# Optimization experiments

Measured on AMD Instinct MI355X. Metric: run time of the kernel, lower is better.

## Reference

```python
import jax, jax.numpy as jnp
import numpy as np

E = 1_000_000   # number of multicut edges
T = 2_000_000   # number of triplets (GNN nodes)
M = 4_000_000   # number of directed GNN edges among triplets
HID = 32


def gcn_conv(x, edge_index, W, b, n):
    """PyG GCNConv: x' = D^-1/2 (A+I) D^-1/2 (x W) + b, symmetric norm with self-loops."""
    src, dst = edge_index[0], edge_index[1]
    xw = x @ W                                        # [n, out]
    deg = jnp.zeros((n,), xw.dtype).at[dst].add(1.0) + 1.0  # +1 self-loop
    dis = jax.lax.rsqrt(deg)                          # deg^-1/2
    norm = dis[src] * dis[dst]                        # [M]
    msg = xw[src] * norm[:, None]                     # gather + scale
    out = jax.ops.segment_sum(msg, dst, num_segments=n)
    out = out + xw * (dis * dis)[:, None]             # self-loop contribution
    return out + b


def setup_inputs() -> dict:
    key = jax.random.key(0)
    ks = jax.random.split(key, 16)
    inp = {
        "edge_costs": jax.random.normal(ks[0], (E,), jnp.float32),
        "t12": jax.random.normal(ks[1], (T,), jnp.float32),
        "t13": jax.random.normal(ks[2], (T,), jnp.float32),
        "t23": jax.random.normal(ks[3], (T,), jnp.float32),
        "corr_12": jax.random.randint(ks[4], (T,), 0, E),
        "corr_13": jax.random.randint(ks[5], (T,), 0, E),
        "corr_23": jax.random.randint(ks[6], (T,), 0, E),
        # counts >= 1 so the divide is well-defined (as in real triplet decompositions)
        "edge_counter": jax.random.randint(ks[7], (E,), 1, 6).astype(jnp.float32),
        "edge_index": jax.random.randint(ks[8], (2, M), 0, T),
        # GCNConv / Linear parameters (glorot-ish scale)
        "W1": jax.random.normal(ks[9], (3, HID), jnp.float32) * (1.0 / np.sqrt(3)),
        "b1": jnp.zeros((HID,), jnp.float32),
        "W2": jax.random.normal(ks[10], (HID, HID), jnp.float32) * (1.0 / np.sqrt(HID)),
        "b2": jnp.zeros((HID,), jnp.float32),
        "Wout": jax.random.normal(ks[11], (HID, 3), jnp.float32) * (1.0 / np.sqrt(HID)),
        "bout": jnp.zeros((3,), jnp.float32),
    }
    return inp


def reference(edge_costs, t12, t13, t23, corr_12, corr_13, corr_23,
              edge_counter, edge_index, W1, b1, W2, b2, Wout, bout):
    # --- send_messages_to_triplets: gather / divide, then zero covered edges ---
    t12 = t12 + edge_costs[corr_12] / edge_counter[corr_12]
    t13 = t13 + edge_costs[corr_13] / edge_counter[corr_13]
    t23 = t23 + edge_costs[corr_23] / edge_counter[corr_23]
    edge_costs = jnp.where(edge_counter > 0, jnp.zeros_like(edge_costs), edge_costs)

    # --- send_messages_to_edges: 2-layer GCN over triplet nodes + linear head ---
    tri = jnp.stack([t12, t13, t23], axis=1)          # [T, 3]
    x = jax.nn.relu(gcn_conv(tri, edge_index, W1, b1, T))
    x = jax.nn.relu(gcn_conv(x, edge_index, W2, b2, T))
    delta = x @ Wout + bout                           # [T, 3]

    t12 = t12 - delta[:, 0]
    t13 = t13 - delta[:, 1]
    t23 = t23 - delta[:, 2]

    edge_updates = (jnp.zeros_like(edge_costs)
                    .at[corr_12].add(delta[:, 0])
                    .at[corr_13].add(delta[:, 1])
                    .at[corr_23].add(delta[:, 2]))
    edge_costs = edge_costs + edge_updates
    return (edge_costs, t12, t13, t23)
```

## Files before the change

### kernel.cpp

```cpp
#include <hip/hip_runtime.h>
#include <hip/hip_fp16.h>
#include <math.h>

#define HID 32
#define BS 256

#define NPB 4096
#define NBK_MAX 1024
#define EBT 8192
#define CAP 11776

typedef _Float16 h2v __attribute__((ext_vector_type(2)));

__device__ __forceinline__ h2v u2h(uint u) { return __builtin_bit_cast(h2v, u); }
__device__ __forceinline__ uint h2u(h2v h) { return __builtin_bit_cast(uint, h); }
__device__ __forceinline__ uint pack2(float a, float b) {
  h2v r; r.x = (_Float16)a; r.y = (_Float16)b; return h2u(r);
}
__device__ __forceinline__ float dot2acc(uint a, uint b, float c) {
#if __has_builtin(__builtin_amdgcn_fdot2)
  return __builtin_amdgcn_fdot2(u2h(a), u2h(b), c, false);
#else
  h2v ah = u2h(a), bh = u2h(b);
  c = fmaf((float)ah.x, (float)bh.x, c);
  return fmaf((float)ah.y, (float)bh.y, c);
#endif
}
__device__ __forceinline__ float h4w(uint2 g) {
  h2v hi = u2h(g.y); return (float)hi.y;
}


__global__ void k_zero_i(int* __restrict__ p, int n) {
  int i = blockIdx.x * BS + threadIdx.x;
  if (i < n) p[i] = 0;
}


__global__ __launch_bounds__(BS) void k_bhist(const int* __restrict__ ei,
                                              int* __restrict__ gh, int M, int NBK) {
  __shared__ int hist[NBK_MAX];
  for (int b = threadIdx.x; b < NBK; b += BS) hist[b] = 0;
  __syncthreads();
  int e0 = blockIdx.x * EBT;
  int n = min(EBT, M - e0);
  for (int k = threadIdx.x; k < n; k += BS) {
    int d = ei[M + e0 + k];
    atomicAdd(&hist[d / NPB], 1);
  }
  __syncthreads();
  for (int b = threadIdx.x; b < NBK; b += BS)
    if (hist[b]) atomicAdd(&gh[b], hist[b]);
}


__global__ __launch_bounds__(BS) void k_bscan(const int* __restrict__ gh,
                                              int* __restrict__ gboff,
                                              int* __restrict__ gcur, int NBK) {
  __shared__ int part[BS];
  int C = (NBK + BS - 1) / BS;
  int s = 0;
  for (int k = 0; k < C; ++k) {
    int idx = threadIdx.x * C + k;
    if (idx < NBK) s += gh[idx];
  }
  part[threadIdx.x] = s;
  __syncthreads();
  for (int off = 1; off < BS; off <<= 1) {
    int v = part[threadIdx.x];
    int u = (threadIdx.x >= off) ? part[threadIdx.x - off] : 0;
    __syncthreads();
    part[threadIdx.x] = v + u;
    __syncthreads();
  }
  int run = (threadIdx.x > 0) ? part[threadIdx.x - 1] : 0;
  for (int k = 0; k < C; ++k) {
    int idx = threadIdx.x * C + k;
    if (idx < NBK) {
      gboff[idx] = run;
      gcur[idx] = run;
      run += gh[idx];
    }
  }
  if (threadIdx.x == BS - 1) gboff[NBK] = run;
}


__global__ __launch_bounds__(BS) void k_bscatter(const int* __restrict__ ei,
                                                 int* __restrict__ gcur,
                                                 int2* __restrict__ P, int M, int NBK) {
  __shared__ int hist[NBK_MAX];
  __shared__ int excl[NBK_MAX];
  __shared__ int curs[NBK_MAX];
  __shared__ int base[NBK_MAX];
  __shared__ int part[BS];
  for (int b = threadIdx.x; b < NBK; b += BS) hist[b] = 0;
  __syncthreads();
  int e0 = blockIdx.x * EBT;
  int n = min(EBT, M - e0);
  for (int k = threadIdx.x; k < n; k += BS) {
    int d = ei[M + e0 + k];
    atomicAdd(&hist[d / NPB], 1);
  }
  __syncthreads();
  int C = (NBK + BS - 1) / BS;
  int s = 0;
  for (int k = 0; k < C; ++k) {
    int idx = threadIdx.x * C + k;
    if (idx < NBK) s += hist[idx];
  }
  part[threadIdx.x] = s;
  __syncthreads();
  for (int off = 1; off < BS; off <<= 1) {
    int v = part[threadIdx.x];
    int u = (threadIdx.x >= off) ? part[threadIdx.x - off] : 0;
    __syncthreads();
    part[threadIdx.x] = v + u;
    __syncthreads();
  }
  int run = (threadIdx.x > 0) ? part[threadIdx.x - 1] : 0;
  for (int k = 0; k < C; ++k) {
    int idx = threadIdx.x * C + k;
    if (idx < NBK) {
      excl[idx] = run;
      curs[idx] = run;
      run += hist[idx];
    }
  }
  __syncthreads();
  for (int b = threadIdx.x; b < NBK; b += BS)
    base[b] = hist[b] ? atomicAdd(&gcur[b], hist[b]) : 0;
  __syncthreads();
  for (int k = threadIdx.x; k < n; k += BS) {
    int sidx = ei[e0 + k];
    int d = ei[M + e0 + k];
    int b = d / NPB;
    int pos = atomicAdd(&curs[b], 1);
    int gpos = base[b] + (pos - excl[b]);
    P[gpos] = make_int2(sidx, d);
  }
}


__global__ __launch_bounds__(BS) void k_bfinal(const int2* __restrict__ P,
                                               const int* __restrict__ gboff,
                                               int* __restrict__ row_ptr,
                                               int* __restrict__ srt, int T, int M,
                                               int NBK) {
  __shared__ int cnt[NPB];
  __shared__ int lsrt[CAP];
  __shared__ int part[BS];
  int b = blockIdx.x;
  int d0 = b * NPB;
  int nodesHere = min(NPB, T - d0);
  int p0 = gboff[b], p1 = gboff[b + 1];
  int nE = p1 - p0;
  for (int j = threadIdx.x; j < NPB; j += BS) cnt[j] = 0;
  __syncthreads();
  for (int j = threadIdx.x; j < nE; j += BS) {
    int2 p = P[p0 + j];
    atomicAdd(&cnt[p.y - d0], 1);
  }
  __syncthreads();
  const int CN = NPB / BS;
  int s = 0;
#pragma unroll
  for (int k = 0; k < CN; ++k) s += cnt[threadIdx.x * CN + k];
  part[threadIdx.x] = s;
  __syncthreads();
  for (int off = 1; off < BS; off <<= 1) {
    int v = part[threadIdx.x];
    int u = (threadIdx.x >= off) ? part[threadIdx.x - off] : 0;
    __syncthreads();
    part[threadIdx.x] = v + u;
    __syncthreads();
  }
  int run = (threadIdx.x > 0) ? part[threadIdx.x - 1] : 0;
#pragma unroll
  for (int k = 0; k < CN; ++k) {
    int idx = threadIdx.x * CN + k;
    int c = cnt[idx];
    cnt[idx] = run;
    if (idx < nodesHere) row_ptr[d0 + idx] = p0 + run;
    run += c;
  }
  if (b == NBK - 1 && threadIdx.x == 0) row_ptr[T] = M;
  __syncthreads();
  if (nE <= CAP) {
    for (int j = threadIdx.x; j < nE; j += BS) {
      int2 p = P[p0 + j];
      int pos = atomicAdd(&cnt[p.y - d0], 1);
      lsrt[pos] = p.x;
    }
    __syncthreads();
    for (int j = threadIdx.x; j < nE; j += BS) srt[p0 + j] = lsrt[j];
  } else {
    for (int j = threadIdx.x; j < nE; j += BS) {
      int2 p = P[p0 + j];
      int pos = atomicAdd(&cnt[p.y - d0], 1);
      srt[p0 + pos] = p.x;
    }
  }
}


__global__ void k_prep_e(const float* __restrict__ ec, const float* __restrict__ cnt,
                         float* __restrict__ msg, float* __restrict__ oec, int E) {
  int i = blockIdx.x * BS + threadIdx.x;
  if (i >= E) return;
  float c = cnt[i], v = ec[i];
  msg[i] = v / c;
  oec[i] = (c > 0.0f) ? 0.0f : v;
}

__global__ void k_step1pack(const float* __restrict__ msg,
                            const float* __restrict__ t12, const float* __restrict__ t13,
                            const float* __restrict__ t23,
                            const int* __restrict__ c12, const int* __restrict__ c13,
                            const int* __restrict__ c23,
                            const int* __restrict__ row_ptr,
                            float4* __restrict__ tri4, uint2* __restrict__ trih, int T) {
  int i = blockIdx.x * BS + threadIdx.x;
  if (i >= T) return;
  int a = c12[i], b = c13[i], c = c23[i];
  float4 v;
  v.x = t12[i] + msg[a];
  v.y = t13[i] + msg[b];
  v.z = t23[i] + msg[c];
  v.w = rsqrtf((float)(row_ptr[i + 1] - row_ptr[i]) + 1.0f);
  tri4[i] = v;
  uint2 h;
  h.x = pack2(v.x, v.y);
  h.y = pack2(v.z, v.w);
  trih[i] = h;
}

__global__ void k_packw(const float* __restrict__ W1, const float* __restrict__ b1,
                        const float* __restrict__ W2, uint* __restrict__ pkw) {
  int i = blockIdx.x * BS + threadIdx.x;
  if (i < 48) {
    int r = i >> 4, k = i & 15;
    pkw[i] = pack2(W1[r * HID + 2 * k], W1[r * HID + 2 * k + 1]);
  } else if (i < 64) {
    int k = i - 48;
    pkw[i] = pack2(b1[2 * k], b1[2 * k + 1]);
  } else if (i < 576) {
    int idx = i - 64;
    int h2 = idx >> 5, j = idx & 31;
    pkw[i] = pack2(W2[(2 * h2) * HID + j], W2[(2 * h2 + 1) * HID + j]);
  }
}

__device__ __forceinline__ void acc3(uint2 g, float di, float& ax, float& ay, float& az) {
  h2v lo = u2h(g.x), hi = u2h(g.y);
  float w = (float)hi.y * di;
  ax = fmaf((float)lo.x, w, ax);
  ay = fmaf((float)lo.y, w, ay);
  az = fmaf((float)hi.x, w, az);
}

__global__ __launch_bounds__(BS) void k_agg1c(const int* __restrict__ row_ptr,
                                              const int* __restrict__ srt,
                                              const float4* __restrict__ tri4,
                                              const uint2* __restrict__ trih,
                                              uint2* __restrict__ G4h, int T) {
  int i = blockIdx.x * BS + threadIdx.x;
  if (i >= T) return;
  int r0 = row_ptr[i], r1 = row_ptr[i + 1];
  float4 ts = tri4[i];
  float di = ts.w;
  float d2 = di * di;
  float ax = ts.x * d2, ay = ts.y * d2, az = ts.z * d2;
  int e = r0;
  for (; e + 4 <= r1; e += 4) {
    int s0 = srt[e + 0];
    int s1 = srt[e + 1];
    int s2 = srt[e + 2];
    int s3 = srt[e + 3];
    uint2 g0 = trih[s0];
    uint2 g1 = trih[s1];
    uint2 g2 = trih[s2];
    uint2 g3 = trih[s3];
    acc3(g0, di, ax, ay, az);
    acc3(g1, di, ax, ay, az);
    acc3(g2, di, ax, ay, az);
    acc3(g3, di, ax, ay, az);
  }
  for (; e < r1; ++e) {
    uint2 g = trih[srt[e]];
    acc3(g, di, ax, ay, az);
  }
  uint2 o;
  o.x = pack2(ax, ay);
  o.y = pack2(az, di);
  G4h[i] = o;
}

__device__ __forceinline__ void edge_h1_accu(uint2 g, float w,
                                             const uint* __restrict__ W1s,
                                             const uint* __restrict__ b1s,
                                             float* S) {
  h2v lo = u2h(g.x), hi = u2h(g.y);
  h2v hx; hx.x = lo.x; hx.y = lo.x;
  h2v hy; hy.x = lo.y; hy.y = lo.y;
  h2v hz; hz.x = hi.x; hz.y = hi.x;
  h2v zero; zero.x = (_Float16)0.f; zero.y = (_Float16)0.f;
#pragma unroll
  for (int k = 0; k < 16; ++k) {
    h2v t = hx * u2h(W1s[k]) + (hy * u2h(W1s[16 + k]) + (hz * u2h(W1s[32 + k]) + u2h(b1s[k])));
    t = __builtin_elementwise_max(t, zero);
    S[2 * k]     = fmaf((float)t.x, w, S[2 * k]);
    S[2 * k + 1] = fmaf((float)t.y, w, S[2 * k + 1]);
  }
}

__global__ __launch_bounds__(BS, 4) void k_l2head(
    const int* __restrict__ row_ptr, const int* __restrict__ srt,
    const uint2* __restrict__ G4h, const float4* __restrict__ tri4,
    const uint* __restrict__ pkw,
    const float* __restrict__ b2,
    const float* __restrict__ Wout, const float* __restrict__ bout,
    const int* __restrict__ c12, const int* __restrict__ c13,
    const int* __restrict__ c23,
    float* __restrict__ o12, float* __restrict__ o13, float* __restrict__ o23,
    float* __restrict__ oec, int T) {
  int i = blockIdx.x * BS + threadIdx.x;
  if (i >= T) return;
  int r0 = row_ptr[i], r1 = row_ptr[i + 1];
  uint2 gs = G4h[i];
  float4 tp = tri4[i];
  float di = tp.w;
  const uint* W1s = pkw;
  const uint* b1s = pkw + 48;
  const uint* W2s = pkw + 64;

  float S[HID];
#pragma unroll
  for (int h = 0; h < HID; ++h) S[h] = 0.0f;

  edge_h1_accu(gs, di * di, W1s, b1s, S);

  int e = r0;
  for (; e + 4 <= r1; e += 4) {
    int s0 = srt[e + 0];
    int s1 = srt[e + 1];
    int s2 = srt[e + 2];
    int s3 = srt[e + 3];
    uint2 g0 = G4h[s0];
    uint2 g1 = G4h[s1];
    uint2 g2 = G4h[s2];
    uint2 g3 = G4h[s3];
    float w0 = h4w(g0) * di;
    float w1 = h4w(g1) * di;
    float w2 = h4w(g2) * di;
    float w3 = h4w(g3) * di;
    edge_h1_accu(g0, w0, W1s, b1s, S);
    edge_h1_accu(g1, w1, W1s, b1s, S);
    edge_h1_accu(g2, w2, W1s, b1s, S);
    edge_h1_accu(g3, w3, W1s, b1s, S);
  }
  if (e + 2 <= r1) {
    int s0 = srt[e + 0];
    int s1 = srt[e + 1];
    uint2 g0 = G4h[s0];
    uint2 g1 = G4h[s1];
    float w0 = h4w(g0) * di;
    float w1 = h4w(g1) * di;
    edge_h1_accu(g0, w0, W1s, b1s, S);
    edge_h1_accu(g1, w1, W1s, b1s, S);
    e += 2;
  }
  if (e < r1) {
    uint2 g = G4h[srt[e]];
    edge_h1_accu(g, h4w(g) * di, W1s, b1s, S);
  }

  uint sh[16];
#pragma unroll
  for (int k = 0; k < 16; ++k) sh[k] = pack2(S[2 * k], S[2 * k + 1]);

  float d0 = bout[0], d1 = bout[1], dd2 = bout[2];
#pragma unroll
  for (int cz = 0; cz < 4; ++cz) {
    float z[8];
#pragma unroll
    for (int j = 0; j < 8; ++j) z[j] = b2[cz * 8 + j];
#pragma unroll
    for (int h2 = 0; h2 < 16; ++h2) {
#pragma unroll
      for (int j = 0; j < 8; ++j)
        z[j] = dot2acc(sh[h2], W2s[h2 * HID + cz * 8 + j], z[j]);
    }
#pragma unroll
    for (int j = 0; j < 8; ++j) {
      float v = fmaxf(z[j], 0.0f);
      int jp = cz * 8 + j;
      d0  = fmaf(v, Wout[jp * 3 + 0], d0);
      d1  = fmaf(v, Wout[jp * 3 + 1], d1);
      dd2 = fmaf(v, Wout[jp * 3 + 2], dd2);
    }
  }

  o12[i] = tp.x - d0;
  o13[i] = tp.y - d1;
  o23[i] = tp.z - dd2;
  unsafeAtomicAdd(&oec[c12[i]], d0);
  unsafeAtomicAdd(&oec[c13[i]], d1);
  unsafeAtomicAdd(&oec[c23[i]], dd2);
}


extern "C" void kernel_launch(void* const* d_in, const int* in_sizes, int n_in,
                              void* d_out, int out_size, void* d_ws, size_t ws_size,
                              hipStream_t stream) {
  const float* ec  = (const float*)d_in[0];
  const float* t12 = (const float*)d_in[1];
  const float* t13 = (const float*)d_in[2];
  const float* t23 = (const float*)d_in[3];
  const int* c12   = (const int*)d_in[4];
  const int* c13   = (const int*)d_in[5];
  const int* c23   = (const int*)d_in[6];
  const float* cnt = (const float*)d_in[7];
  const int* ei    = (const int*)d_in[8];
  const float* W1  = (const float*)d_in[9];
  const float* b1  = (const float*)d_in[10];
  const float* W2  = (const float*)d_in[11];
  const float* b2  = (const float*)d_in[12];
  const float* Wout = (const float*)d_in[13];
  const float* bout = (const float*)d_in[14];

  const int E = in_sizes[0];
  const int T = in_sizes[1];
  const int M = in_sizes[8] / 2;
  const int NBK = (T + NPB - 1) / NPB;

  float* oec = (float*)d_out;
  float* o12 = oec + E;
  float* o13 = o12 + T;
  float* o23 = o13 + T;

  float4* tri4 = (float4*)d_ws;
  uint2*  trih = (uint2*)(tri4 + T);
  uint2*  G4h  = trih + T;
  int*    srt  = (int*)(G4h + T);
  int*    rptr = srt + M;
  float*  msg  = (float*)(rptr + (T + 1));
  int*    gh   = (int*)(msg + E);
  int*    gboff = gh + NBK;
  int*    gcur  = gboff + (NBK + 1);
  uint*   pkw   = (uint*)(gcur + NBK);
  int2*   P    = (int2*)tri4;

  auto blocks = [](long n) { return (int)((n + BS - 1) / BS); };
  const int tiles = (M + EBT - 1) / EBT;

  k_zero_i<<<blocks(NBK), BS, 0, stream>>>(gh, NBK);
  k_bhist<<<tiles, BS, 0, stream>>>(ei, gh, M, NBK);
  k_bscan<<<1, BS, 0, stream>>>(gh, gboff, gcur, NBK);
  k_bscatter<<<tiles, BS, 0, stream>>>(ei, gcur, P, M, NBK);
  k_bfinal<<<NBK, BS, 0, stream>>>(P, gboff, rptr, srt, T, M, NBK);

  k_packw<<<3, BS, 0, stream>>>(W1, b1, W2, pkw);
  k_prep_e<<<blocks(E), BS, 0, stream>>>(ec, cnt, msg, oec, E);
  k_step1pack<<<blocks(T), BS, 0, stream>>>(msg, t12, t13, t23, c12, c13, c23,
                                            rptr, tri4, trih, T);

  k_agg1c<<<blocks(T), BS, 0, stream>>>(rptr, srt, tri4, trih, G4h, T);

  k_l2head<<<blocks(T), BS, 0, stream>>>(rptr, srt, G4h, tri4, pkw,
                                         b2, Wout, bout,
                                         c12, c13, c23, o12, o13, o23, oec, T);
}
```

Baseline: 709.1 us.

## Replace global atomic edge scatter with bucketed sort and shared-memory segment sum

The per-triplet global float atomics into the edge cost array are removed. The head kernel now writes deltas to a buffer, and the 3T (edge, triplet) pairs are bucket-sorted by edge index into 1024-edge bins. A new kernel then gathers and accumulates each bin with shared-memory atomics and does a single coalesced add into the output. This adds four extra launches plus histogram and scatter passes over 6M keys, and the launch-bounds occupancy hint on the head kernel is dropped.

```diff
diff --git a/kernel.cpp b/kernel.cpp
--- a/kernel.cpp
+++ b/kernel.cpp
@@ -9,6 +9,8 @@
 #define NBK_MAX 1024
 #define EBT 8192
 #define CAP 11776
+
+#define NPB_E 1024
 
 typedef _Float16 h2v __attribute__((ext_vector_type(2)));
 
@@ -201,6 +203,121 @@
       srt[p0 + pos] = p.x;
     }
   }
+}
+
+
+__global__ __launch_bounds__(BS) void k_ehist(const int* __restrict__ c12,
+                                              const int* __restrict__ c13,
+                                              const int* __restrict__ c23,
+                                              int* __restrict__ gh, int T, int NBK) {
+  __shared__ int hist[NBK_MAX];
+  for (int b = threadIdx.x; b < NBK; b += BS) hist[b] = 0;
+  __syncthreads();
+  int N3 = 3 * T;
+  int j0 = blockIdx.x * EBT;
+  int n = min(EBT, N3 - j0);
+  for (int k = threadIdx.x; k < n; k += BS) {
+    int j = j0 + k;
+    int key = (j < T) ? c12[j] : ((j < 2 * T) ? c13[j - T] : c23[j - 2 * T]);
+    atomicAdd(&hist[key / NPB_E], 1);
+  }
+  __syncthreads();
+  for (int b = threadIdx.x; b < NBK; b += BS)
+    if (hist[b]) atomicAdd(&gh[b], hist[b]);
+}
+
+__global__ __launch_bounds__(BS) void k_escatter(const int* __restrict__ c12,
+                                                 const int* __restrict__ c13,
+                                                 const int* __restrict__ c23,
+                                                 int* __restrict__ gcur,
+                                                 int2* __restrict__ PE, int T, int NBK) {
+  __shared__ int hist[NBK_MAX];
+  __shared__ int excl[NBK_MAX];
+  __shared__ int curs[NBK_MAX];
+  __shared__ int base[NBK_MAX];
+  __shared__ int part[BS];
+  for (int b = threadIdx.x; b < NBK; b += BS) hist[b] = 0;
+  __syncthreads();
+  int N3 = 3 * T;
+  int j0 = blockIdx.x * EBT;
+  int n = min(EBT, N3 - j0);
+  for (int k = threadIdx.x; k < n; k += BS) {
+    int j = j0 + k;
+    int key = (j < T) ? c12[j] : ((j < 2 * T) ? c13[j - T] : c23[j - 2 * T]);
+    atomicAdd(&hist[key / NPB_E], 1);
+  }
+  __syncthreads();
+  int C = (NBK + BS - 1) / BS;
+  int s = 0;
+  for (int k = 0; k < C; ++k) {
+    int idx = threadIdx.x * C + k;
+    if (idx < NBK) s += hist[idx];
+  }
+  part[threadIdx.x] = s;
+  __syncthreads();
+  for (int off = 1; off < BS; off <<= 1) {
+    int v = part[threadIdx.x];
+    int u = (threadIdx.x >= off) ? part[threadIdx.x - off] : 0;
+    __syncthreads();
+    part[threadIdx.x] = v + u;
+    __syncthreads();
+  }
+  int run = (threadIdx.x > 0) ? part[threadIdx.x - 1] : 0;
+  for (int k = 0; k < C; ++k) {
+    int idx = threadIdx.x * C + k;
+    if (idx < NBK) {
+      excl[idx] = run;
+      curs[idx] = run;
+      run += hist[idx];
+    }
+  }
+  __syncthreads();
+  for (int b = threadIdx.x; b < NBK; b += BS)
+    base[b] = hist[b] ? atomicAdd(&gcur[b], hist[b]) : 0;
+  __syncthreads();
+  for (int k = threadIdx.x; k < n; k += BS) {
+    int j = j0 + k;
+    int key = (j < T) ? c12[j] : ((j < 2 * T) ? c13[j - T] : c23[j - 2 * T]);
+    int b = key / NPB_E;
+    int pos = atomicAdd(&curs[b], 1);
+    int gpos = base[b] + (pos - excl[b]);
+    PE[gpos] = make_int2(key, j);
+  }
+}
+
+__global__ __launch_bounds__(BS) void k_oecsum(const int2* __restrict__ PE,
+                                               const int* __restrict__ gboff,
+                                               const float* __restrict__ dd,
+                                               float* __restrict__ oec, int E) {
+  __shared__ float acc[NPB_E];
+  int b = blockIdx.x;
+  int e0 = b * NPB_E;
+  int p0 = gboff[b], p1 = gboff[b + 1];
+  int n = p1 - p0;
+  for (int j = threadIdx.x; j < NPB_E; j += BS) acc[j] = 0.0f;
+  __syncthreads();
+  int k = threadIdx.x;
+  for (; k + 3 * BS < n; k += 4 * BS) {
+    int2 q0 = PE[p0 + k];
+    int2 q1 = PE[p0 + k + BS];
+    int2 q2 = PE[p0 + k + 2 * BS];
+    int2 q3 = PE[p0 + k + 3 * BS];
+    float v0 = dd[q0.y];
+    float v1 = dd[q1.y];
+    float v2 = dd[q2.y];
+    float v3 = dd[q3.y];
+    atomicAdd(&acc[q0.x - e0], v0);
+    atomicAdd(&acc[q1.x - e0], v1);
+    atomicAdd(&acc[q2.x - e0], v2);
+    atomicAdd(&acc[q3.x - e0], v3);
+  }
+  for (; k < n; k += BS) {
+    int2 q = PE[p0 + k];
+    atomicAdd(&acc[q.x - e0], dd[q.y]);
+  }
+  __syncthreads();
+  int lim = min(NPB_E, E - e0);
+  for (int j = threadIdx.x; j < lim; j += BS) oec[e0 + j] += acc[j];
 }
 
 
@@ -314,16 +431,14 @@
   }
 }
 
-__global__ __launch_bounds__(BS, 4) void k_l2head(
+__global__ __launch_bounds__(BS) void k_l2head(
     const int* __restrict__ row_ptr, const int* __restrict__ srt,
     const uint2* __restrict__ G4h, const float4* __restrict__ tri4,
     const uint* __restrict__ pkw,
     const float* __restrict__ b2,
     const float* __restrict__ Wout, const float* __restrict__ bout,
-    const int* __restrict__ c12, const int* __restrict__ c13,
-    const int* __restrict__ c23,
     float* __restrict__ o12, float* __restrict__ o13, float* __restrict__ o23,
-    float* __restrict__ oec, int T) {
+    float* __restrict__ dd, int T) {
   int i = blockIdx.x * BS + threadIdx.x;
   if (i >= T) return;
   int r0 = row_ptr[i], r1 = row_ptr[i + 1];
@@ -404,9 +519,9 @@
   o12[i] = tp.x - d0;
   o13[i] = tp.y - d1;
   o23[i] = tp.z - dd2;
-  unsafeAtomicAdd(&oec[c12[i]], d0);
-  unsafeAtomicAdd(&oec[c13[i]], d1);
-  unsafeAtomicAdd(&oec[c23[i]], dd2);
+  dd[i] = d0;
+  dd[T + i] = d1;
+  dd[2 * T + i] = dd2;
 }
 
 
@@ -433,6 +548,7 @@
   const int T = in_sizes[1];
   const int M = in_sizes[8] / 2;
   const int NBK = (T + NPB - 1) / NPB;
+  const int NBK_E = (E + NPB_E - 1) / NPB_E;
 
   float* oec = (float*)d_out;
   float* o12 = oec + E;
@@ -442,17 +558,23 @@
   float4* tri4 = (float4*)d_ws;
   uint2*  trih = (uint2*)(tri4 + T);
   uint2*  G4h  = trih + T;
-  int*    srt  = (int*)(G4h + T);
+  int2*   PE   = (int2*)(G4h + T);
+  float*  dd   = (float*)(PE + 3 * (size_t)T);
+  int*    srt  = (int*)(dd + 3 * (size_t)T);
   int*    rptr = srt + M;
   float*  msg  = (float*)(rptr + (T + 1));
   int*    gh   = (int*)(msg + E);
   int*    gboff = gh + NBK;
   int*    gcur  = gboff + (NBK + 1);
   uint*   pkw   = (uint*)(gcur + NBK);
+  int*    gh_e  = (int*)(pkw + 576);
+  int*    gboff_e = gh_e + NBK_E;
+  int*    gcur_e  = gboff_e + (NBK_E + 1);
   int2*   P    = (int2*)tri4;
 
   auto blocks = [](long n) { return (int)((n + BS - 1) / BS); };
-  const int tiles = (M + EBT - 1) / EBT;
+  const int tiles   = (M + EBT - 1) / EBT;
+  const int tiles_e = (3 * T + EBT - 1) / EBT;
 
   k_zero_i<<<blocks(NBK), BS, 0, stream>>>(gh, NBK);
   k_bhist<<<tiles, BS, 0, stream>>>(ei, gh, M, NBK);
@@ -460,6 +582,11 @@
   k_bscatter<<<tiles, BS, 0, stream>>>(ei, gcur, P, M, NBK);
   k_bfinal<<<NBK, BS, 0, stream>>>(P, gboff, rptr, srt, T, M, NBK);
 
+  k_zero_i<<<blocks(NBK_E), BS, 0, stream>>>(gh_e, NBK_E);
+  k_ehist<<<tiles_e, BS, 0, stream>>>(c12, c13, c23, gh_e, T, NBK_E);
+  k_bscan<<<1, BS, 0, stream>>>(gh_e, gboff_e, gcur_e, NBK_E);
+  k_escatter<<<tiles_e, BS, 0, stream>>>(c12, c13, c23, gcur_e, PE, T, NBK_E);
+
   k_packw<<<3, BS, 0, stream>>>(W1, b1, W2, pkw);
   k_prep_e<<<blocks(E), BS, 0, stream>>>(ec, cnt, msg, oec, E);
   k_step1pack<<<blocks(T), BS, 0, stream>>>(msg, t12, t13, t23, c12, c13, c23,
@@ -469,5 +596,7 @@
 
   k_l2head<<<blocks(T), BS, 0, stream>>>(rptr, srt, G4h, tri4, pkw,
                                          b2, Wout, bout,
-                                         c12, c13, c23, o12, o13, o23, oec, T);
-}
+                                         o12, o13, o23, dd, T);
+
+  k_oecsum<<<NBK_E, BS, 0, stream>>>(PE, gboff_e, dd, oec, E);
+}
```

Measured after the change: 718.4 us. About the same (+1.3%).

## Replace global scatter-add atomics with bucketed sort and shared-memory reduction

Applied to the files above, without the earlier changes.

The final edge-cost scatter-add no longer uses random global atomics from the GCN head. The head now writes deltas to a buffer, which is bucket-sorted by edge index using per-tile histograms and then reduced per bucket with shared-memory atomics. The node-sort pipeline is also rebuilt around deterministic per-tile offsets, replacing the global cursor atomics and the zeroing kernel. The launch-bounds occupancy hint on k_l2head is dropped as well. The cost is extra passes over 6M keys and values, several more kernel launches, and more workspace.

```diff
diff --git a/kernel.cpp b/kernel.cpp
--- a/kernel.cpp
+++ b/kernel.cpp
@@ -9,6 +9,8 @@
 #define NBK_MAX 1024
 #define EBT 8192
 #define CAP 11776
+
+#define NPB_E 2048
 
 typedef _Float16 h2v __attribute__((ext_vector_type(2)));
 
@@ -31,14 +33,8 @@
 }
 
 
-__global__ void k_zero_i(int* __restrict__ p, int n) {
-  int i = blockIdx.x * BS + threadIdx.x;
-  if (i < n) p[i] = 0;
-}
-
-
-__global__ __launch_bounds__(BS) void k_bhist(const int* __restrict__ ei,
-                                              int* __restrict__ gh, int M, int NBK) {
+__global__ __launch_bounds__(BS) void k_bhist2(const int* __restrict__ ei,
+                                               int* __restrict__ thist, int M, int NBK) {
   __shared__ int hist[NBK_MAX];
   for (int b = threadIdx.x; b < NBK; b += BS) hist[b] = 0;
   __syncthreads();
@@ -50,9 +46,60 @@
   }
   __syncthreads();
   for (int b = threadIdx.x; b < NBK; b += BS)
-    if (hist[b]) atomicAdd(&gh[b], hist[b]);
-}
-
+    thist[blockIdx.x * NBK + b] = hist[b];
+}
+
+__global__ __launch_bounds__(BS) void k_ehist2(const int* __restrict__ c12,
+                                               const int* __restrict__ c13,
+                                               const int* __restrict__ c23,
+                                               int* __restrict__ thist, int T, int NBK) {
+  __shared__ int hist[NBK_MAX];
+  for (int b = threadIdx.x; b < NBK; b += BS) hist[b] = 0;
+  __syncthreads();
+  int N3 = 3 * T;
+  int j0 = blockIdx.x * EBT;
+  int n = min(EBT, N3 - j0);
+  for (int k = threadIdx.x; k < n; k += BS) {
+    int j = j0 + k;
+    int key = (j < T) ? c12[j] : ((j < 2 * T) ? c13[j - T] : c23[j - 2 * T]);
+    atomicAdd(&hist[key / NPB_E], 1);
+  }
+  __syncthreads();
+  for (int b = threadIdx.x; b < NBK; b += BS)
+    thist[blockIdx.x * NBK + b] = hist[b];
+}
+
+__global__ __launch_bounds__(BS) void k_tbase(const int* __restrict__ thist,
+                                              int* __restrict__ tbase,
+                                              int* __restrict__ gh, int NBK, int NT) {
+  __shared__ int part[BS];
+  int b = blockIdx.x;
+  int C = (NT + BS - 1) / BS;
+  int s = 0;
+  for (int k = 0; k < C; ++k) {
+    int t = threadIdx.x * C + k;
+    if (t < NT) s += thist[t * NBK + b];
+  }
+  part[threadIdx.x] = s;
+  __syncthreads();
+  for (int off = 1; off < BS; off <<= 1) {
+    int v = part[threadIdx.x];
+    int u = (threadIdx.x >= off) ? part[threadIdx.x - off] : 0;
+    __syncthreads();
+    part[threadIdx.x] = v + u;
+    __syncthreads();
+  }
+  int run = (threadIdx.x > 0) ? part[threadIdx.x - 1] : 0;
+  for (int k = 0; k < C; ++k) {
+    int t = threadIdx.x * C + k;
+    if (t < NT) {
+      int v = thist[t * NBK + b];
+      tbase[t * NBK + b] = run;
+      run += v;
+    }
+  }
+  if (threadIdx.x == BS - 1) gh[b] = run;
+}
 
 __global__ __launch_bounds__(BS) void k_bscan(const int* __restrict__ gh,
                                               int* __restrict__ gboff,
@@ -85,59 +132,46 @@
   if (threadIdx.x == BS - 1) gboff[NBK] = run;
 }
 
-
-__global__ __launch_bounds__(BS) void k_bscatter(const int* __restrict__ ei,
-                                                 int* __restrict__ gcur,
-                                                 int2* __restrict__ P, int M, int NBK) {
-  __shared__ int hist[NBK_MAX];
-  __shared__ int excl[NBK_MAX];
-  __shared__ int curs[NBK_MAX];
-  __shared__ int base[NBK_MAX];
-  __shared__ int part[BS];
-  for (int b = threadIdx.x; b < NBK; b += BS) hist[b] = 0;
-  __syncthreads();
-  int e0 = blockIdx.x * EBT;
+__global__ __launch_bounds__(BS) void k_bplace(const int* __restrict__ ei,
+                                               const int* __restrict__ gboff,
+                                               const int* __restrict__ tbase,
+                                               int2* __restrict__ P, int M, int NBK) {
+  __shared__ int cur[NBK_MAX];
+  int t = blockIdx.x;
+  for (int b = threadIdx.x; b < NBK; b += BS)
+    cur[b] = gboff[b] + tbase[t * NBK + b];
+  __syncthreads();
+  int e0 = t * EBT;
   int n = min(EBT, M - e0);
-  for (int k = threadIdx.x; k < n; k += BS) {
-    int d = ei[M + e0 + k];
-    atomicAdd(&hist[d / NPB], 1);
-  }
-  __syncthreads();
-  int C = (NBK + BS - 1) / BS;
-  int s = 0;
-  for (int k = 0; k < C; ++k) {
-    int idx = threadIdx.x * C + k;
-    if (idx < NBK) s += hist[idx];
-  }
-  part[threadIdx.x] = s;
-  __syncthreads();
-  for (int off = 1; off < BS; off <<= 1) {
-    int v = part[threadIdx.x];
-    int u = (threadIdx.x >= off) ? part[threadIdx.x - off] : 0;
-    __syncthreads();
-    part[threadIdx.x] = v + u;
-    __syncthreads();
-  }
-  int run = (threadIdx.x > 0) ? part[threadIdx.x - 1] : 0;
-  for (int k = 0; k < C; ++k) {
-    int idx = threadIdx.x * C + k;
-    if (idx < NBK) {
-      excl[idx] = run;
-      curs[idx] = run;
-      run += hist[idx];
-    }
-  }
-  __syncthreads();
-  for (int b = threadIdx.x; b < NBK; b += BS)
-    base[b] = hist[b] ? atomicAdd(&gcur[b], hist[b]) : 0;
-  __syncthreads();
   for (int k = threadIdx.x; k < n; k += BS) {
     int sidx = ei[e0 + k];
     int d = ei[M + e0 + k];
-    int b = d / NPB;
-    int pos = atomicAdd(&curs[b], 1);
-    int gpos = base[b] + (pos - excl[b]);
-    P[gpos] = make_int2(sidx, d);
+    int pos = atomicAdd(&cur[d / NPB], 1);
+    P[pos] = make_int2(sidx, d);
+  }
+}
+
+__global__ __launch_bounds__(BS) void k_escatv(const int* __restrict__ c12,
+                                               const int* __restrict__ c13,
+                                               const int* __restrict__ c23,
+                                               const float* __restrict__ dd,
+                                               const int* __restrict__ gboff,
+                                               const int* __restrict__ tbase,
+                                               int2* __restrict__ PEV, int T, int NBK) {
+  __shared__ int cur[NBK_MAX];
+  int t = blockIdx.x;
+  for (int b = threadIdx.x; b < NBK; b += BS)
+    cur[b] = gboff[b] + tbase[t * NBK + b];
+  __syncthreads();
+  int N3 = 3 * T;
+  int j0 = t * EBT;
+  int n = min(EBT, N3 - j0);
+  for (int k = threadIdx.x; k < n; k += BS) {
+    int j = j0 + k;
+    int key = (j < T) ? c12[j] : ((j < 2 * T) ? c13[j - T] : c23[j - 2 * T]);
+    float v = dd[j];
+    int pos = atomicAdd(&cur[key / NPB_E], 1);
+    PEV[pos] = make_int2(key, __builtin_bit_cast(int, v));
   }
 }
 
@@ -201,6 +235,36 @@
       srt[p0 + pos] = p.x;
     }
   }
+}
+
+__global__ __launch_bounds__(BS) void k_oecsum2(const int2* __restrict__ PEV,
+                                                const int* __restrict__ gboff,
+                                                float* __restrict__ oec, int E) {
+  __shared__ float acc[NPB_E];
+  int b = blockIdx.x;
+  int e0 = b * NPB_E;
+  int p0 = gboff[b], p1 = gboff[b + 1];
+  int n = p1 - p0;
+  for (int j = threadIdx.x; j < NPB_E; j += BS) acc[j] = 0.0f;
+  __syncthreads();
+  int k = threadIdx.x;
+  for (; k + 3 * BS < n; k += 4 * BS) {
+    int2 q0 = PEV[p0 + k];
+    int2 q1 = PEV[p0 + k + BS];
+    int2 q2 = PEV[p0 + k + 2 * BS];
+    int2 q3 = PEV[p0 + k + 3 * BS];
+    atomicAdd(&acc[q0.x - e0], __builtin_bit_cast(float, q0.y));
+    atomicAdd(&acc[q1.x - e0], __builtin_bit_cast(float, q1.y));
+    atomicAdd(&acc[q2.x - e0], __builtin_bit_cast(float, q2.y));
+    atomicAdd(&acc[q3.x - e0], __builtin_bit_cast(float, q3.y));
+  }
+  for (; k < n; k += BS) {
+    int2 q = PEV[p0 + k];
+    atomicAdd(&acc[q.x - e0], __builtin_bit_cast(float, q.y));
+  }
+  __syncthreads();
+  int lim = min(NPB_E, E - e0);
+  for (int j = threadIdx.x; j < lim; j += BS) oec[e0 + j] += acc[j];
 }
 
 
@@ -314,16 +378,14 @@
   }
 }
 
-__global__ __launch_bounds__(BS, 4) void k_l2head(
+__global__ __launch_bounds__(BS) void k_l2head(
     const int* __restrict__ row_ptr, const int* __restrict__ srt,
     const uint2* __restrict__ G4h, const float4* __restrict__ tri4,
     const uint* __restrict__ pkw,
     const float* __restrict__ b2,
     const float* __restrict__ Wout, const float* __restrict__ bout,
-    const int* __restrict__ c12, const int* __restrict__ c13,
-    const int* __restrict__ c23,
     float* __restrict__ o12, float* __restrict__ o13, float* __restrict__ o23,
-    float* __restrict__ oec, int T) {
+    float* __restrict__ dd, int T) {
   int i = blockIdx.x * BS + threadIdx.x;
   if (i >= T) return;
   int r0 = row_ptr[i], r1 = row_ptr[i + 1];
@@ -404,9 +466,9 @@
   o12[i] = tp.x - d0;
   o13[i] = tp.y - d1;
   o23[i] = tp.z - dd2;
-  unsafeAtomicAdd(&oec[c12[i]], d0);
-  unsafeAtomicAdd(&oec[c13[i]], d1);
-  unsafeAtomicAdd(&oec[c23[i]], dd2);
+  dd[i] = d0;
+  dd[T + i] = d1;
+  dd[2 * T + i] = dd2;
 }
 
 
@@ -433,32 +495,47 @@
   const int T = in_sizes[1];
   const int M = in_sizes[8] / 2;
   const int NBK = (T + NPB - 1) / NPB;
+  const int NBK_E = (E + NPB_E - 1) / NPB_E;
 
   float* oec = (float*)d_out;
   float* o12 = oec + E;
   float* o13 = o12 + T;
   float* o23 = o13 + T;
 
+  auto blocks = [](long n) { return (int)((n + BS - 1) / BS); };
+  const int tiles   = (M + EBT - 1) / EBT;
+  const int tiles_e = (3 * T + EBT - 1) / EBT;
+
   float4* tri4 = (float4*)d_ws;
   uint2*  trih = (uint2*)(tri4 + T);
   uint2*  G4h  = trih + T;
-  int*    srt  = (int*)(G4h + T);
+  int2*   PEV  = (int2*)(G4h + T);
+  float*  dd   = (float*)(PEV + 3 * (size_t)T);
+  int*    srt  = (int*)(dd + 3 * (size_t)T);
   int*    rptr = srt + M;
   float*  msg  = (float*)(rptr + (T + 1));
   int*    gh   = (int*)(msg + E);
   int*    gboff = gh + NBK;
   int*    gcur  = gboff + (NBK + 1);
   uint*   pkw   = (uint*)(gcur + NBK);
+  int*    gh_e  = (int*)(pkw + 576);
+  int*    gboff_e = gh_e + NBK_E;
+  int*    gcur_e  = gboff_e + (NBK_E + 1);
+  int*    thist_n = gcur_e + NBK_E;
+  int*    tbase_n = thist_n + (size_t)tiles * NBK;
+  int*    thist_e = tbase_n + (size_t)tiles * NBK;
+  int*    tbase_e = thist_e + (size_t)tiles_e * NBK_E;
   int2*   P    = (int2*)tri4;
 
-  auto blocks = [](long n) { return (int)((n + BS - 1) / BS); };
-  const int tiles = (M + EBT - 1) / EBT;
-
-  k_zero_i<<<blocks(NBK), BS, 0, stream>>>(gh, NBK);
-  k_bhist<<<tiles, BS, 0, stream>>>(ei, gh, M, NBK);
+  k_bhist2<<<tiles, BS, 0, stream>>>(ei, thist_n, M, NBK);
+  k_tbase<<<NBK, BS, 0, stream>>>(thist_n, tbase_n, gh, NBK, tiles);
   k_bscan<<<1, BS, 0, stream>>>(gh, gboff, gcur, NBK);
-  k_bscatter<<<tiles, BS, 0, stream>>>(ei, gcur, P, M, NBK);
+  k_bplace<<<tiles, BS, 0, stream>>>(ei, gboff, tbase_n, P, M, NBK);
   k_bfinal<<<NBK, BS, 0, stream>>>(P, gboff, rptr, srt, T, M, NBK);
+
+  k_ehist2<<<tiles_e, BS, 0, stream>>>(c12, c13, c23, thist_e, T, NBK_E);
+  k_tbase<<<NBK_E, BS, 0, stream>>>(thist_e, tbase_e, gh_e, NBK_E, tiles_e);
+  k_bscan<<<1, BS, 0, stream>>>(gh_e, gboff_e, gcur_e, NBK_E);
 
   k_packw<<<3, BS, 0, stream>>>(W1, b1, W2, pkw);
   k_prep_e<<<blocks(E), BS, 0, stream>>>(ec, cnt, msg, oec, E);
@@ -469,5 +546,9 @@
 
   k_l2head<<<blocks(T), BS, 0, stream>>>(rptr, srt, G4h, tri4, pkw,
                                          b2, Wout, bout,
-                                         c12, c13, c23, o12, o13, o23, oec, T);
-}
+                                         o12, o13, o23, dd, T);
+
+  k_escatv<<<tiles_e, BS, 0, stream>>>(c12, c13, c23, dd, gboff_e, tbase_e,
+                                       PEV, T, NBK_E);
+  k_oecsum2<<<NBK_E, BS, 0, stream>>>(PEV, gboff_e, oec, E);
+}
```

Measured after the change: 618.3 us. 1.15x faster.
